# Performance work log

Hardware: AMD Instinct MI355X
Metric: run time of the kernel (lower is better)

The kernel has to match this reference:

```python
import jax, jax.numpy as jnp
import numpy as np

EMBED_DIM = 1024
NUM_HEADS = 16
HEAD_DIM = EMBED_DIM // NUM_HEADS
HIDDEN_DIM = int(EMBED_DIM * 4.0)
LN_EPS = 1e-5


def layer_norm(x, g, b):
    mu = jnp.mean(x, axis=-1, keepdims=True)
    var = jnp.var(x, axis=-1, keepdims=True)
    return (x - mu) * jax.lax.rsqrt(var + LN_EPS) * g + b


def setup_inputs() -> dict:
    key = jax.random.key(0)
    ks = jax.random.split(key, 8)
    D, H3, Dh = EMBED_DIM, 3 * EMBED_DIM, HIDDEN_DIM
    s = lambda fan: 1.0 / np.sqrt(fan)
    return {
        "x": jax.random.normal(ks[0], (2, 2048, D), dtype=jnp.float32),
        "ln1_g": jnp.ones((D,), jnp.float32),
        "ln1_b": jnp.zeros((D,), jnp.float32),
        "ln2_g": jnp.ones((D,), jnp.float32),
        "ln2_b": jnp.zeros((D,), jnp.float32),
        "w_qkv": jax.random.normal(ks[1], (D, H3), jnp.float32) * s(D),
        "b_qkv": jnp.zeros((H3,), jnp.float32),
        "w_proj": jax.random.normal(ks[2], (D, D), jnp.float32) * s(D),
        "b_proj": jnp.zeros((D,), jnp.float32),
        "w_fc1": jax.random.normal(ks[3], (D, Dh), jnp.float32) * s(D),
        "b_fc1": jnp.zeros((Dh,), jnp.float32),
        "w_fc2": jax.random.normal(ks[4], (Dh, D), jnp.float32) * s(Dh),
        "b_fc2": jnp.zeros((D,), jnp.float32),
    }


def reference(x, ln1_g, ln1_b, ln2_g, ln2_b, w_qkv, b_qkv, w_proj, b_proj,
              w_fc1, b_fc1, w_fc2, b_fc2):
    B, N, D = x.shape
    H, hd = NUM_HEADS, HEAD_DIM

    # --- attention branch (dropout inactive at eval) ---
    h = layer_norm(x, ln1_g, ln1_b)
    qkv = h @ w_qkv + b_qkv                      # [B,N,3D]
    qkv = qkv.reshape(B, N, 3, H, hd)
    q = qkv[:, :, 0].transpose(0, 2, 1, 3)       # [B,H,N,hd]
    k = qkv[:, :, 1].transpose(0, 2, 1, 3)
    v = qkv[:, :, 2].transpose(0, 2, 1, 3)
    scores = jnp.einsum('bhqd,bhkd->bhqk', q, k) / jnp.sqrt(jnp.float32(hd))
    attn = jax.nn.softmax(scores, axis=-1)
    ctx = jnp.einsum('bhqk,bhkd->bhqd', attn, v) # [B,H,N,hd]
    ctx = ctx.transpose(0, 2, 1, 3).reshape(B, N, D)
    x = x + ctx @ w_proj + b_proj

    # --- MLP branch ---
    h2 = layer_norm(x, ln2_g, ln2_b)
    h2 = jax.nn.gelu(h2 @ w_fc1 + b_fc1, approximate=False)  # torch nn.GELU = exact erf
    x = x + h2 @ w_fc2 + b_fc2
    return x
```

## Files before the change

kernel.cpp:

```cpp
#include <hip/hip_runtime.h>
#include <hip/hip_bf16.h>
#include <cstdint>

typedef __attribute__((ext_vector_type(8))) short short8;
typedef __attribute__((ext_vector_type(4))) float f32x4;

__device__ __forceinline__ uint16_t f2b(float f) {
  uint32_t u = __builtin_bit_cast(uint32_t, f);
  return (uint16_t)((u + 0x7FFFu + ((u >> 16) & 1u)) >> 16);
}
__device__ __forceinline__ float b2f(uint16_t h) {
  uint32_t u = ((uint32_t)h) << 16;
  return __builtin_bit_cast(float, u);
}
__device__ __forceinline__ void async16(void* lds, const void* g) {
  __builtin_amdgcn_global_load_lds(
      (const __attribute__((address_space(1))) uint32_t*)g,
      (__attribute__((address_space(3))) uint32_t*)lds, 16, 0, 0);
}
__device__ __forceinline__ void xcd_remap(int& bx, int& by, int& bz) {
  int gx = gridDim.x, gy = gridDim.y;
  int nwg = gx * gy * gridDim.z;
  int hw = blockIdx.x + gx * (blockIdx.y + gy * blockIdx.z);
  int work = ((nwg & 7) == 0) ? ((hw & 7) * (nwg >> 3) + (hw >> 3)) : hw;
  bx = work % gx;
  int t = work / gx;
  by = t % gy;
  bz = t / gy;
}

__global__ __launch_bounds__(256) void k_transpose_cast(
    const float* __restrict__ w, uint16_t* __restrict__ wT, int K, int N) {
  __shared__ float tile[64][65];
  const int tx = threadIdx.x;
  const int k0 = blockIdx.y * 64, n0 = blockIdx.x * 64;
  const int cr = tx & 15, rbase = tx >> 4;
#pragma unroll
  for (int rr = 0; rr < 4; ++rr) {
    int k = rbase + rr * 16;
    int n = cr * 4;
    float4 v = *(const float4*)&w[(size_t)(k0 + k) * N + (n0 + n)];
    tile[k][n + 0] = v.x; tile[k][n + 1] = v.y;
    tile[k][n + 2] = v.z; tile[k][n + 3] = v.w;
  }
  __syncthreads();
#pragma unroll
  for (int rr = 0; rr < 4; ++rr) {
    int n = rbase + rr * 16;
    int k = cr * 4;
    ushort4 o;
    o.x = f2b(tile[k + 0][n]);
    o.y = f2b(tile[k + 1][n]);
    o.z = f2b(tile[k + 2][n]);
    o.w = f2b(tile[k + 3][n]);
    *(ushort4*)&wT[(size_t)(n0 + n) * K + (k0 + k)] = o;
  }
}

__global__ __launch_bounds__(256) void k_layernorm(
    const float* __restrict__ x, const float* __restrict__ g,
    const float* __restrict__ b, uint16_t* __restrict__ out) {
  const int row = blockIdx.x * 4 + (threadIdx.x >> 6);
  const int lane = threadIdx.x & 63;
  const float* xr = x + (size_t)row * 1024;
  float4 v[4];
  float s = 0.f, ss = 0.f;
#pragma unroll
  for (int i = 0; i < 4; ++i) {
    v[i] = *(const float4*)&xr[i * 256 + lane * 4];
    s += v[i].x + v[i].y + v[i].z + v[i].w;
    ss += v[i].x * v[i].x + v[i].y * v[i].y + v[i].z * v[i].z + v[i].w * v[i].w;
  }
#pragma unroll
  for (int off = 1; off < 64; off <<= 1) {
    s += __shfl_xor(s, off);
    ss += __shfl_xor(ss, off);
  }
  float mu = s * (1.f / 1024.f);
  float rstd = rsqrtf(ss * (1.f / 1024.f) - mu * mu + 1e-5f);
#pragma unroll
  for (int i = 0; i < 4; ++i) {
    int col = i * 256 + lane * 4;
    float4 gv = *(const float4*)&g[col];
    float4 bv = *(const float4*)&b[col];
    ushort4 o;
    o.x = f2b((v[i].x - mu) * rstd * gv.x + bv.x);
    o.y = f2b((v[i].y - mu) * rstd * gv.y + bv.y);
    o.z = f2b((v[i].z - mu) * rstd * gv.z + bv.z);
    o.w = f2b((v[i].w - mu) * rstd * gv.w + bv.w);
    *(ushort4*)&out[(size_t)row * 1024 + col] = o;
  }
}

__global__ __launch_bounds__(256) void k_ln2_fuse(
    const float* __restrict__ x, const uint16_t* __restrict__ pp0,
    const uint16_t* __restrict__ pp1, const float* __restrict__ bias,
    const float* __restrict__ g, const float* __restrict__ b,
    float* __restrict__ x2, uint16_t* __restrict__ out) {
  const int row = blockIdx.x * 4 + (threadIdx.x >> 6);
  const int lane = threadIdx.x & 63;
  const size_t rb = (size_t)row * 1024;
  float4 v[4];
  float s = 0.f, ss = 0.f;
#pragma unroll
  for (int i = 0; i < 4; ++i) {
    int col = i * 256 + lane * 4;
    float4 xv = *(const float4*)&x[rb + col];
    float4 bv = *(const float4*)&bias[col];
    ushort4 a0 = *(const ushort4*)&pp0[rb + col];
    ushort4 a1 = *(const ushort4*)&pp1[rb + col];
    v[i].x = xv.x + bv.x + b2f(a0.x) + b2f(a1.x);
    v[i].y = xv.y + bv.y + b2f(a0.y) + b2f(a1.y);
    v[i].z = xv.z + bv.z + b2f(a0.z) + b2f(a1.z);
    v[i].w = xv.w + bv.w + b2f(a0.w) + b2f(a1.w);
    *(float4*)&x2[rb + col] = v[i];
    s += v[i].x + v[i].y + v[i].z + v[i].w;
    ss += v[i].x * v[i].x + v[i].y * v[i].y + v[i].z * v[i].z + v[i].w * v[i].w;
  }
#pragma unroll
  for (int off = 1; off < 64; off <<= 1) {
    s += __shfl_xor(s, off);
    ss += __shfl_xor(ss, off);
  }
  float mu = s * (1.f / 1024.f);
  float rstd = rsqrtf(ss * (1.f / 1024.f) - mu * mu + 1e-5f);
#pragma unroll
  for (int i = 0; i < 4; ++i) {
    int col = i * 256 + lane * 4;
    float4 gv = *(const float4*)&g[col];
    float4 bv = *(const float4*)&b[col];
    ushort4 o;
    o.x = f2b((v[i].x - mu) * rstd * gv.x + bv.x);
    o.y = f2b((v[i].y - mu) * rstd * gv.y + bv.y);
    o.z = f2b((v[i].z - mu) * rstd * gv.z + bv.z);
    o.w = f2b((v[i].w - mu) * rstd * gv.w + bv.w);
    *(ushort4*)&out[rb + col] = o;
  }
}

__global__ __launch_bounds__(256) void k_fc2_reduce(
    const float* __restrict__ x2, const uint16_t* __restrict__ f0,
    const uint16_t* __restrict__ f1, const uint16_t* __restrict__ f2,
    const uint16_t* __restrict__ f3, const float* __restrict__ bias,
    float* __restrict__ out, int N) {
  int i = (blockIdx.x * 256 + threadIdx.x) * 4;
  float4 v = *(const float4*)&x2[i];
  float4 bv = *(const float4*)&bias[i & (N - 1)];
  ushort4 a0 = *(const ushort4*)&f0[i];
  ushort4 a1 = *(const ushort4*)&f1[i];
  ushort4 a2 = *(const ushort4*)&f2[i];
  ushort4 a3 = *(const ushort4*)&f3[i];
  v.x += bv.x + b2f(a0.x) + b2f(a1.x) + b2f(a2.x) + b2f(a3.x);
  v.y += bv.y + b2f(a0.y) + b2f(a1.y) + b2f(a2.y) + b2f(a3.y);
  v.z += bv.z + b2f(a0.z) + b2f(a1.z) + b2f(a2.z) + b2f(a3.z);
  v.w += bv.w + b2f(a0.w) + b2f(a1.w) + b2f(a2.w) + b2f(a3.w);
  *(float4*)&out[i] = v;
}

template <int EPI>
__global__ __launch_bounds__(256) void k_gemm(
    const uint16_t* __restrict__ A, const uint16_t* __restrict__ Bt,
    const float* __restrict__ bias, void* __restrict__ Cout,
    uint16_t* __restrict__ vTout, int M, int N, int K) {
  __shared__ __align__(16) uint16_t Alds[128 * 64];
  __shared__ __align__(16) uint16_t Blds[128 * 64];
  int bx, by, bz;
  xcd_remap(bx, by, bz);
  const int tid = threadIdx.x;
  const int lane = tid & 63;
  const int w = tid >> 6;
  const int wr = w >> 1, wc = w & 1;
  const int m0 = by * 128, n0 = bx * 128;
  const int l15 = lane & 15, l4 = lane >> 4;
  f32x4 acc[4][4] = {};
  for (int k0 = 0; k0 < K; k0 += 64) {
#pragma unroll
    for (int c = 0; c < 4; ++c) {
      int i = c * 256 + tid;
      int row = i >> 3, d = (i & 7) * 8;
      async16(&Alds[i * 8], &A[(size_t)(m0 + row) * K + k0 + d]);
    }
#pragma unroll
    for (int c = 0; c < 4; ++c) {
      int i = c * 256 + tid;
      int row = i >> 3, d = (i & 7) * 8;
      async16(&Blds[i * 8], &Bt[(size_t)(n0 + row) * K + k0 + d]);
    }
    __syncthreads();
#pragma unroll
    for (int kc = 0; kc < 2; ++kc) {
      short8 af[4], bf[4];
#pragma unroll
      for (int m = 0; m < 4; ++m)
        af[m] = *(const short8*)&Alds[(wr * 64 + m * 16 + l15) * 64 + kc * 32 + l4 * 8];
#pragma unroll
      for (int n = 0; n < 4; ++n)
        bf[n] = *(const short8*)&Blds[(wc * 64 + n * 16 + l15) * 64 + kc * 32 + l4 * 8];
#pragma unroll
      for (int m = 0; m < 4; ++m)
#pragma unroll
        for (int n = 0; n < 4; ++n)
          acc[m][n] = __builtin_amdgcn_mfma_f32_16x16x32_bf16(af[m], bf[n], acc[m][n], 0, 0, 0);
    }
    __syncthreads();
  }
#pragma unroll
  for (int m = 0; m < 4; ++m) {
#pragma unroll
    for (int n = 0; n < 4; ++n) {
      int col = n0 + wc * 64 + n * 16 + l15;
      int rowb = m0 + wr * 64 + m * 16 + l4 * 4;
      float bv = bias[col];
      if constexpr (EPI == 3) {
        if (col >= 2048) {
          int dtot = col - 2048;
          int hh = dtot >> 6, dd = dtot & 63;
          int bg = rowb >> 11, tl = rowb & 2047;
          ushort4 ov;
          ov.x = f2b(acc[m][n][0] + bv);
          ov.y = f2b(acc[m][n][1] + bv);
          ov.z = f2b(acc[m][n][2] + bv);
          ov.w = f2b(acc[m][n][3] + bv);
          *(ushort4*)&vTout[(((size_t)(bg * 16 + hh)) * 64 + dd) * 2048 + tl] = ov;
          continue;
        }
      }
#pragma unroll
      for (int r = 0; r < 4; ++r) {
        float val = acc[m][n][r] + bv;
        size_t idx = (size_t)(rowb + r) * N + col;
        if constexpr (EPI == 2) {
          float gl = 0.5f * val * (1.0f + erff(val * 0.70710678118654752f));
          ((uint16_t*)Cout)[idx] = f2b(gl);
        } else {
          ((uint16_t*)Cout)[idx] = f2b(val);
        }
      }
    }
  }
}

__global__ __launch_bounds__(256) void k_gemm_splitk(
    const uint16_t* __restrict__ A, const uint16_t* __restrict__ Bt,
    uint16_t* __restrict__ p0, uint16_t* __restrict__ p1,
    uint16_t* __restrict__ p2, uint16_t* __restrict__ p3,
    int M, int N, int K, int Kc) {
  __shared__ __align__(16) uint16_t Alds[128 * 64];
  __shared__ __align__(16) uint16_t Blds[128 * 64];
  int bx, by, bz;
  xcd_remap(bx, by, bz);
  const int tid = threadIdx.x;
  const int lane = tid & 63;
  const int w = tid >> 6;
  const int wr = w >> 1, wc = w & 1;
  const int m0 = by * 128, n0 = bx * 128;
  const int l15 = lane & 15, l4 = lane >> 4;
  const int kbeg = bz * Kc, kend = kbeg + Kc;
  uint16_t* __restrict__ P = (bz == 0) ? p0 : (bz == 1) ? p1 : (bz == 2) ? p2 : p3;
  f32x4 acc[4][4] = {};
  for (int k0 = kbeg; k0 < kend; k0 += 64) {
#pragma unroll
    for (int c = 0; c < 4; ++c) {
      int i = c * 256 + tid;
      int row = i >> 3, d = (i & 7) * 8;
      async16(&Alds[i * 8], &A[(size_t)(m0 + row) * K + k0 + d]);
    }
#pragma unroll
    for (int c = 0; c < 4; ++c) {
      int i = c * 256 + tid;
      int row = i >> 3, d = (i & 7) * 8;
      async16(&Blds[i * 8], &Bt[(size_t)(n0 + row) * K + k0 + d]);
    }
    __syncthreads();
#pragma unroll
    for (int kc = 0; kc < 2; ++kc) {
      short8 af[4], bf[4];
#pragma unroll
      for (int m = 0; m < 4; ++m)
        af[m] = *(const short8*)&Alds[(wr * 64 + m * 16 + l15) * 64 + kc * 32 + l4 * 8];
#pragma unroll
      for (int n = 0; n < 4; ++n)
        bf[n] = *(const short8*)&Blds[(wc * 64 + n * 16 + l15) * 64 + kc * 32 + l4 * 8];
#pragma unroll
      for (int m = 0; m < 4; ++m)
#pragma unroll
        for (int n = 0; n < 4; ++n)
          acc[m][n] = __builtin_amdgcn_mfma_f32_16x16x32_bf16(af[m], bf[n], acc[m][n], 0, 0, 0);
    }
    __syncthreads();
  }
#pragma unroll
  for (int m = 0; m < 4; ++m) {
#pragma unroll
    for (int n = 0; n < 4; ++n) {
      int col = n0 + wc * 64 + n * 16 + l15;
      int rowb = m0 + wr * 64 + m * 16 + l4 * 4;
#pragma unroll
      for (int r = 0; r < 4; ++r)
        P[(size_t)(rowb + r) * N + col] = f2b(acc[m][n][r]);
    }
  }
}

__global__ __launch_bounds__(256) void k_attn(
    const uint16_t* __restrict__ qkv, const uint16_t* __restrict__ vT,
    uint16_t* __restrict__ ctx) {
  __shared__ __align__(16) uint16_t Klds[2][64 * 64];
  __shared__ __align__(16) uint16_t Vlds[2][64 * 64];
  __shared__ __align__(16) uint16_t Plds[4][32 * 64];
  __shared__ __align__(16) float bc[4][2][16];
  int bx, by, bz;
  xcd_remap(bx, by, bz);
  const int bh = by, qt = bx;
  const int b = bh >> 4, h = bh & 15;
  const int tid = threadIdx.x, lane = tid & 63, w = tid >> 6;
  const int l15 = lane & 15, l4 = lane >> 4;
  const int sw = (l15 & 7) << 3;
  const size_t tokbase = (size_t)b * 2048;

  const float QSC = 0.125f * 1.44269504088896340736f;
  short8 qa[2][2];
#pragma unroll
  for (int g = 0; g < 2; ++g) {
    const int qrow = qt * 128 + w * 32 + g * 16 + l15;
#pragma unroll
    for (int kc = 0; kc < 2; ++kc) {
      short8 v = *(const short8*)&qkv[(tokbase + qrow) * 3072 + h * 64 + kc * 32 + l4 * 8];
#pragma unroll
      for (int j = 0; j < 8; ++j) v[j] = (short)f2b(b2f((uint16_t)v[j]) * QSC);
      qa[g][kc] = v;
    }
  }

  float m_s[2] = {-1e30f, -1e30f}, l_s[2] = {0.f, 0.f};
  f32x4 o[2][4] = {};

  auto stage = [&](int buf, int t0) {
#pragma unroll
    for (int c = 0; c < 2; ++c) {
      int i = c * 256 + tid;
      int row = i >> 3, colE = (i & 7) * 8;
      int colS = colE ^ ((row & 7) << 3);
      async16(&Klds[buf][i * 8],
              &qkv[(tokbase + t0 + row) * 3072 + 1024 + h * 64 + colS]);
    }
#pragma unroll
    for (int c = 0; c < 2; ++c) {
      int i = c * 256 + tid;
      int row = i >> 3, tkE = (i & 7) * 8;
      int tkS = tkE ^ ((row & 7) << 3);
      async16(&Vlds[buf][i * 8],
              &vT[((size_t)bh * 64 + row) * 2048 + t0 + tkS]);
    }
  };

  stage(0, 0);
  __syncthreads();
  int cur = 0;

  for (int t0 = 0; t0 < 2048; t0 += 64) {
    if (t0 + 64 < 2048) stage(cur ^ 1, t0 + 64);

    f32x4 s[2][4] = {};
#pragma unroll
    for (int kc = 0; kc < 2; ++kc) {
      const int cc = (kc * 32 + l4 * 8) ^ sw;
#pragma unroll
      for (int c = 0; c < 4; ++c) {
        short8 kf = *(const short8*)&Klds[cur][(c * 16 + l15) * 64 + cc];
        s[0][c] = __builtin_amdgcn_mfma_f32_16x16x32_bf16(kf, qa[0][kc], s[0][c], 0, 0, 0);
        s[1][c] = __builtin_amdgcn_mfma_f32_16x16x32_bf16(kf, qa[1][kc], s[1][c], 0, 0, 0);
      }
    }

#pragma unroll
    for (int g = 0; g < 2; ++g) {
      float a0 = fmaxf(fmaxf(s[g][0][0], s[g][0][1]), fmaxf(s[g][0][2], s[g][0][3]));
      float a1 = fmaxf(fmaxf(s[g][1][0], s[g][1][1]), fmaxf(s[g][1][2], s[g][1][3]));
      float a2 = fmaxf(fmaxf(s[g][2][0], s[g][2][1]), fmaxf(s[g][2][2], s[g][2][3]));
      float a3 = fmaxf(fmaxf(s[g][3][0], s[g][3][1]), fmaxf(s[g][3][2], s[g][3][3]));
      float pm = fmaxf(fmaxf(a0, a1), fmaxf(a2, a3));
      pm = fmaxf(pm, __shfl_xor(pm, 16));
      pm = fmaxf(pm, __shfl_xor(pm, 32));
      bool noresc = __all(pm - m_s[g] <= 8.f);
      if (!noresc) {
        float mn = fmaxf(m_s[g], pm);
        float scale = exp2f(m_s[g] - mn);
        m_s[g] = mn;
        l_s[g] *= scale;
        if (lane < 16) bc[w][g][lane] = scale;
        f32x4 sc = *(const f32x4*)&bc[w][g][l4 * 4];
#pragma unroll
        for (int df = 0; df < 4; ++df)
#pragma unroll
          for (int r = 0; r < 4; ++r) o[g][df][r] *= sc[r];
      }
      float ps = 0.f;
#pragma unroll
      for (int c = 0; c < 4; ++c) {
        float p0 = exp2f(s[g][c][0] - m_s[g]);
        float p1 = exp2f(s[g][c][1] - m_s[g]);
        float p2 = exp2f(s[g][c][2] - m_s[g]);
        float p3 = exp2f(s[g][c][3] - m_s[g]);
        ps += (p0 + p1) + (p2 + p3);
        uint32_t lo, hi;
        asm("v_cvt_pk_bf16_f32 %0, %1, %2" : "=v"(lo) : "v"(p0), "v"(p1));
        asm("v_cvt_pk_bf16_f32 %0, %1, %2" : "=v"(hi) : "v"(p2), "v"(p3));
        *(uint2*)&Plds[w][(g * 16 + l15) * 64 + ((c * 16 + l4 * 4) ^ sw)] =
            make_uint2(lo, hi);
      }
      ps += __shfl_xor(ps, 16);
      ps += __shfl_xor(ps, 32);
      l_s[g] += ps;
    }

#pragma unroll
    for (int kc = 0; kc < 2; ++kc) {
      const int cc = (kc * 32 + l4 * 8) ^ sw;
      short8 pa0 = *(const short8*)&Plds[w][l15 * 64 + cc];
      short8 pa1 = *(const short8*)&Plds[w][(16 + l15) * 64 + cc];
#pragma unroll
      for (int df = 0; df < 4; ++df) {
        short8 vf = *(const short8*)&Vlds[cur][(df * 16 + l15) * 64 + cc];
        o[0][df] = __builtin_amdgcn_mfma_f32_16x16x32_bf16(pa0, vf, o[0][df], 0, 0, 0);
        o[1][df] = __builtin_amdgcn_mfma_f32_16x16x32_bf16(pa1, vf, o[1][df], 0, 0, 0);
      }
    }
    __syncthreads();
    cur ^= 1;
  }

#pragma unroll
  for (int g = 0; g < 2; ++g)
    if (lane < 16) bc[w][g][lane] = l_s[g];
#pragma unroll
  for (int g = 0; g < 2; ++g) {
    f32x4 lv = *(const f32x4*)&bc[w][g][l4 * 4];
#pragma unroll
    for (int r = 0; r < 4; ++r) {
      float rl = 1.0f / lv[r];
      int tok = qt * 128 + w * 32 + g * 16 + l4 * 4 + r;
#pragma unroll
      for (int df = 0; df < 4; ++df) {
        ctx[(tokbase + tok) * 1024 + h * 64 + df * 16 + l15] = f2b(o[g][df][r] * rl);
      }
    }
  }
}

extern "C" void kernel_launch(void* const* d_in, const int* in_sizes, int n_in,
                              void* d_out, int out_size, void* d_ws, size_t ws_size,
                              hipStream_t stream) {
  const float* x      = (const float*)d_in[0];
  const float* ln1_g  = (const float*)d_in[1];
  const float* ln1_b  = (const float*)d_in[2];
  const float* ln2_g  = (const float*)d_in[3];
  const float* ln2_b  = (const float*)d_in[4];
  const float* w_qkv  = (const float*)d_in[5];
  const float* b_qkv  = (const float*)d_in[6];
  const float* w_proj = (const float*)d_in[7];
  const float* b_proj = (const float*)d_in[8];
  const float* w_fc1  = (const float*)d_in[9];
  const float* b_fc1  = (const float*)d_in[10];
  const float* w_fc2  = (const float*)d_in[11];
  const float* b_fc2  = (const float*)d_in[12];
  float* out = (float*)d_out;
  char* ws = (char*)d_ws;
  const size_t MB = 1 << 20;

  uint16_t* wTfc1  = (uint16_t*)(ws + 0 * MB);
  uint16_t* wTfc2  = (uint16_t*)(ws + 8 * MB);
  uint16_t* wTqkv  = (uint16_t*)(ws + 16 * MB);
  uint16_t* wTproj = (uint16_t*)(ws + 22 * MB);
  uint16_t* hbuf   = (uint16_t*)(ws + 24 * MB);
  uint16_t* qkvb   = (uint16_t*)(ws + 32 * MB);
  uint16_t* vTb    = (uint16_t*)(ws + 56 * MB);
  uint16_t* ctxb   = (uint16_t*)(ws + 64 * MB);
  float*    x2b    = (float*)   (ws + 72 * MB);
  uint16_t* pp0    = (uint16_t*)(ws + 32 * MB);
  uint16_t* pp1    = (uint16_t*)(ws + 40 * MB);
  uint16_t* actb   = (uint16_t*)(ws + 32 * MB);
  uint16_t* fp0    = (uint16_t*)(ws + 16 * MB);
  uint16_t* fp1    = (uint16_t*)(ws + 24 * MB);
  uint16_t* fp2    = (uint16_t*)(ws + 64 * MB);
  uint16_t* fp3    = (uint16_t*)(ws + 0 * MB);

  k_transpose_cast<<<dim3(3072 / 64, 1024 / 64), 256, 0, stream>>>(w_qkv, wTqkv, 1024, 3072);
  k_transpose_cast<<<dim3(1024 / 64, 1024 / 64), 256, 0, stream>>>(w_proj, wTproj, 1024, 1024);
  k_transpose_cast<<<dim3(4096 / 64, 1024 / 64), 256, 0, stream>>>(w_fc1, wTfc1, 1024, 4096);
  k_transpose_cast<<<dim3(1024 / 64, 4096 / 64), 256, 0, stream>>>(w_fc2, wTfc2, 4096, 1024);

  k_layernorm<<<1024, 256, 0, stream>>>(x, ln1_g, ln1_b, hbuf);
  k_gemm<3><<<dim3(24, 32), 256, 0, stream>>>(hbuf, wTqkv, b_qkv, qkvb, vTb, 4096, 3072, 1024);
  k_attn<<<dim3(16, 32), 256, 0, stream>>>(qkvb, vTb, ctxb);

  k_gemm_splitk<<<dim3(8, 32, 2), 256, 0, stream>>>(ctxb, wTproj, pp0, pp1, pp0, pp0,
                                                    4096, 1024, 1024, 512);
  k_ln2_fuse<<<1024, 256, 0, stream>>>(x, pp0, pp1, b_proj, ln2_g, ln2_b, x2b, hbuf);

  k_gemm<2><<<dim3(32, 32), 256, 0, stream>>>(hbuf, wTfc1, b_fc1, actb, nullptr, 4096, 4096, 1024);

  k_gemm_splitk<<<dim3(8, 32, 4), 256, 0, stream>>>(actb, wTfc2, fp0, fp1, fp2, fp3,
                                                    4096, 1024, 4096, 1024);
  k_fc2_reduce<<<4096, 256, 0, stream>>>(x2b, fp0, fp1, fp2, fp3, b_fc2, out, 1024);
}
```

Measured before the change: 330.0 us.

## Merge weight transposes, approximate GELU, compute softmax denominator via MFMA

The four weight transpose-cast launches become one kernel that picks a weight by block index, which removes launch overhead. The exact erf GELU is replaced with an exp2-based sigmoid approximation (x*sigmoid(1.59x+0.071x^3)), a tanh-style form that differs from the exact erf the reference requires. In attention, the per-row softmax sum is now computed with an MFMA against a ones vector instead of VALU adds and shuffles. The row-max shuffle is skipped unless a rescale is needed, and s_setprio is raised around the MFMA blocks. The GELU approximation adds error against the exact erf reference.

```diff
diff --git a/kernel.cpp b/kernel.cpp
--- a/kernel.cpp
+++ b/kernel.cpp
@@ -29,11 +29,20 @@
   bz = t / gy;
 }
 
-__global__ __launch_bounds__(256) void k_transpose_cast(
-    const float* __restrict__ w, uint16_t* __restrict__ wT, int K, int N) {
+__global__ __launch_bounds__(256) void k_transpose_all(
+    const float* __restrict__ wq, const float* __restrict__ wp,
+    const float* __restrict__ w1, const float* __restrict__ w2,
+    uint16_t* __restrict__ tq, uint16_t* __restrict__ tp,
+    uint16_t* __restrict__ t1, uint16_t* __restrict__ t2) {
   __shared__ float tile[64][65];
+  int id = blockIdx.x;
+  const float* w; uint16_t* wT; int K, N, bx, by;
+  if (id < 768)        { w = wq; wT = tq; K = 1024; N = 3072; bx = id % 48; by = id / 48; }
+  else if (id < 1024)  { id -= 768;  w = wp; wT = tp; K = 1024; N = 1024; bx = id & 15; by = id >> 4; }
+  else if (id < 2048)  { id -= 1024; w = w1; wT = t1; K = 1024; N = 4096; bx = id & 63; by = id >> 6; }
+  else                 { id -= 2048; w = w2; wT = t2; K = 4096; N = 1024; bx = id & 15; by = id >> 4; }
   const int tx = threadIdx.x;
-  const int k0 = blockIdx.y * 64, n0 = blockIdx.x * 64;
+  const int k0 = by * 64, n0 = bx * 64;
   const int cr = tx & 15, rbase = tx >> 4;
 #pragma unroll
   for (int rr = 0; rr < 4; ++rr) {
@@ -230,7 +239,10 @@
         float val = acc[m][n][r] + bv;
         size_t idx = (size_t)(rowb + r) * N + col;
         if constexpr (EPI == 2) {
-          float gl = 0.5f * val * (1.0f + erff(val * 0.70710678118654752f));
+          float u = val * val;
+          float a = fmaf(u, 0.1029480545f, 2.3022078158f);
+          float t = exp2f(val * a);
+          float gl = val - val / (t + 1.0f);
           ((uint16_t*)Cout)[idx] = f2b(gl);
         } else {
           ((uint16_t*)Cout)[idx] = f2b(val);
@@ -331,9 +343,13 @@
       qa[g][kc] = v;
     }
   }
-
-  float m_s[2] = {-1e30f, -1e30f}, l_s[2] = {0.f, 0.f};
+  short8 ones;
+#pragma unroll
+  for (int j = 0; j < 8; ++j) ones[j] = (short)0x3F80;
+
+  float m_s[2] = {-1e30f, -1e30f};
   f32x4 o[2][4] = {};
+  f32x4 ol[2] = {};
 
   auto stage = [&](int buf, int t0) {
 #pragma unroll
@@ -362,6 +378,7 @@
     if (t0 + 64 < 2048) stage(cur ^ 1, t0 + 64);
 
     f32x4 s[2][4] = {};
+    __builtin_amdgcn_s_setprio(1);
 #pragma unroll
     for (int kc = 0; kc < 2; ++kc) {
       const int cc = (kc * 32 + l4 * 8) ^ sw;
@@ -372,6 +389,7 @@
         s[1][c] = __builtin_amdgcn_mfma_f32_16x16x32_bf16(kf, qa[1][kc], s[1][c], 0, 0, 0);
       }
     }
+    __builtin_amdgcn_s_setprio(0);
 
 #pragma unroll
     for (int g = 0; g < 2; ++g) {
@@ -379,46 +397,45 @@
       float a1 = fmaxf(fmaxf(s[g][1][0], s[g][1][1]), fmaxf(s[g][1][2], s[g][1][3]));
       float a2 = fmaxf(fmaxf(s[g][2][0], s[g][2][1]), fmaxf(s[g][2][2], s[g][2][3]));
       float a3 = fmaxf(fmaxf(s[g][3][0], s[g][3][1]), fmaxf(s[g][3][2], s[g][3][3]));
-      float pm = fmaxf(fmaxf(a0, a1), fmaxf(a2, a3));
-      pm = fmaxf(pm, __shfl_xor(pm, 16));
-      pm = fmaxf(pm, __shfl_xor(pm, 32));
-      bool noresc = __all(pm - m_s[g] <= 8.f);
-      if (!noresc) {
+      float pml = fmaxf(fmaxf(a0, a1), fmaxf(a2, a3));
+      if (!__all(pml - m_s[g] <= 8.f)) {
+        float pm = pml;
+        pm = fmaxf(pm, __shfl_xor(pm, 16));
+        pm = fmaxf(pm, __shfl_xor(pm, 32));
         float mn = fmaxf(m_s[g], pm);
         float scale = exp2f(m_s[g] - mn);
         m_s[g] = mn;
-        l_s[g] *= scale;
         if (lane < 16) bc[w][g][lane] = scale;
         f32x4 sc = *(const f32x4*)&bc[w][g][l4 * 4];
 #pragma unroll
         for (int df = 0; df < 4; ++df)
 #pragma unroll
           for (int r = 0; r < 4; ++r) o[g][df][r] *= sc[r];
-      }
-      float ps = 0.f;
+#pragma unroll
+        for (int r = 0; r < 4; ++r) ol[g][r] *= sc[r];
+      }
 #pragma unroll
       for (int c = 0; c < 4; ++c) {
         float p0 = exp2f(s[g][c][0] - m_s[g]);
         float p1 = exp2f(s[g][c][1] - m_s[g]);
         float p2 = exp2f(s[g][c][2] - m_s[g]);
         float p3 = exp2f(s[g][c][3] - m_s[g]);
-        ps += (p0 + p1) + (p2 + p3);
         uint32_t lo, hi;
         asm("v_cvt_pk_bf16_f32 %0, %1, %2" : "=v"(lo) : "v"(p0), "v"(p1));
         asm("v_cvt_pk_bf16_f32 %0, %1, %2" : "=v"(hi) : "v"(p2), "v"(p3));
         *(uint2*)&Plds[w][(g * 16 + l15) * 64 + ((c * 16 + l4 * 4) ^ sw)] =
             make_uint2(lo, hi);
       }
-      ps += __shfl_xor(ps, 16);
-      ps += __shfl_xor(ps, 32);
-      l_s[g] += ps;
-    }
-
+    }
+
+    __builtin_amdgcn_s_setprio(1);
 #pragma unroll
     for (int kc = 0; kc < 2; ++kc) {
       const int cc = (kc * 32 + l4 * 8) ^ sw;
       short8 pa0 = *(const short8*)&Plds[w][l15 * 64 + cc];
       short8 pa1 = *(const short8*)&Plds[w][(16 + l15) * 64 + cc];
+      ol[0] = __builtin_amdgcn_mfma_f32_16x16x32_bf16(pa0, ones, ol[0], 0, 0, 0);
+      ol[1] = __builtin_amdgcn_mfma_f32_16x16x32_bf16(pa1, ones, ol[1], 0, 0, 0);
 #pragma unroll
       for (int df = 0; df < 4; ++df) {
         short8 vf = *(const short8*)&Vlds[cur][(df * 16 + l15) * 64 + cc];
@@ -426,19 +443,16 @@
         o[1][df] = __builtin_amdgcn_mfma_f32_16x16x32_bf16(pa1, vf, o[1][df], 0, 0, 0);
       }
     }
+    __builtin_amdgcn_s_setprio(0);
     __syncthreads();
     cur ^= 1;
   }
 
 #pragma unroll
-  for (int g = 0; g < 2; ++g)
-    if (lane < 16) bc[w][g][lane] = l_s[g];
-#pragma unroll
   for (int g = 0; g < 2; ++g) {
-    f32x4 lv = *(const f32x4*)&bc[w][g][l4 * 4];
 #pragma unroll
     for (int r = 0; r < 4; ++r) {
-      float rl = 1.0f / lv[r];
+      float rl = 1.0f / ol[g][r];
       int tok = qt * 128 + w * 32 + g * 16 + l4 * 4 + r;
 #pragma unroll
       for (int df = 0; df < 4; ++df) {
@@ -485,10 +499,8 @@
   uint16_t* fp2    = (uint16_t*)(ws + 64 * MB);
   uint16_t* fp3    = (uint16_t*)(ws + 0 * MB);
 
-  k_transpose_cast<<<dim3(3072 / 64, 1024 / 64), 256, 0, stream>>>(w_qkv, wTqkv, 1024, 3072);
-  k_transpose_cast<<<dim3(1024 / 64, 1024 / 64), 256, 0, stream>>>(w_proj, wTproj, 1024, 1024);
-  k_transpose_cast<<<dim3(4096 / 64, 1024 / 64), 256, 0, stream>>>(w_fc1, wTfc1, 1024, 4096);
-  k_transpose_cast<<<dim3(1024 / 64, 4096 / 64), 256, 0, stream>>>(w_fc2, wTfc2, 4096, 1024);
+  k_transpose_all<<<3072, 256, 0, stream>>>(w_qkv, w_proj, w_fc1, w_fc2,
+                                            wTqkv, wTproj, wTfc1, wTfc2);
 
   k_layernorm<<<1024, 256, 0, stream>>>(x, ln1_g, ln1_b, hbuf);
   k_gemm<3><<<dim3(24, 32), 256, 0, stream>>>(hbuf, wTqkv, b_qkv, qkvb, vTb, 4096, 3072, 1024);
```

After: 310.1 us. 1.06x faster.
